# Performance work log

Measured on AMD Instinct MI355X. Metric: run time of the kernel, lower is better.

## Reference

```python
import jax, jax.numpy as jnp
import numpy as np

HID = 512
NUM_NODES = 100000
N_BATCH = 20000


def _gru_cell(x, h, W_ih, W_hh, b_ih, b_hh):
    # torch nn.GRU single-step cell; gate order r, z, n
    gi = x @ W_ih.T + b_ih            # [N, 3H]
    gh = h @ W_hh.T + b_hh            # [N, 3H]
    i_r, i_z, i_n = jnp.split(gi, 3, axis=-1)
    h_r, h_z, h_n = jnp.split(gh, 3, axis=-1)
    r = jax.nn.sigmoid(i_r + h_r)
    z = jax.nn.sigmoid(i_z + h_z)
    n = jnp.tanh(i_n + r * h_n)
    return (1.0 - z) * n + z * h


def setup_inputs() -> dict:
    key = jax.random.key(0)
    ks = jax.random.split(key, 12)
    s = 1.0 / np.sqrt(HID)
    inp = {
        'conv_emb': jax.random.normal(ks[0], (N_BATCH, HID), jnp.float32),
        'static_table': jax.random.normal(ks[1], (NUM_NODES, HID), jnp.float32),
        'dynamic_table': jax.random.normal(ks[2], (NUM_NODES, 2, HID), jnp.float32),
        'W_ih0': jax.random.normal(ks[3], (3 * HID, 2 * HID), jnp.float32) * s,
        'W_hh0': jax.random.normal(ks[4], (3 * HID, HID), jnp.float32) * s,
        'b_ih0': jax.random.normal(ks[5], (3 * HID,), jnp.float32) * s,
        'b_hh0': jax.random.normal(ks[6], (3 * HID,), jnp.float32) * s,
        'W_ih1': jax.random.normal(ks[7], (3 * HID, HID), jnp.float32) * s,
        'W_hh1': jax.random.normal(ks[8], (3 * HID, HID), jnp.float32) * s,
        'b_ih1': jax.random.normal(ks[9], (3 * HID,), jnp.float32) * s,
        'b_hh1': jax.random.normal(ks[10], (3 * HID,), jnp.float32) * s,
        'nids': jnp.arange(N_BATCH, dtype=jnp.int32),  # unique global node ids
    }
    return inp


def reference(conv_emb, static_table, dynamic_table,
              W_ih0, W_hh0, b_ih0, b_hh0,
              W_ih1, W_hh1, b_ih1, b_hh1, nids):
    # gather: static embeddings for batch nodes, concat with conv output
    x = jnp.concatenate([conv_emb, static_table[nids]], axis=-1)  # [N, 2H]
    h0 = dynamic_table[nids]                                      # [N, L, H]
    # single-step 2-layer GRU (seq_len == 1)
    h_new0 = _gru_cell(x, h0[:, 0], W_ih0, W_hh0, b_ih0, b_hh0)   # [N, H]
    h_new1 = _gru_cell(h_new0, h0[:, 1], W_ih1, W_hh1, b_ih1, b_hh1)
    hn = jnp.stack([h_new0, h_new1], axis=1)                      # [N, L, H]
    # scatter updated hidden states back into the persistent table
    updated_table = dynamic_table.at[nids].set(hn)                # [num_nodes, L, H]
    return updated_table
```

## Files before the change

### kernel.cpp

```cpp
#include <hip/hip_runtime.h>

#define NB 20000
#define NNODES 100000
#define MB2 79
#define MP2 (MB2*256)
#define NBITW 3125
#define NGEMM (MB2*8)

typedef unsigned short u16;
typedef __bf16 bf16x8 __attribute__((ext_vector_type(8)));
typedef float f32x4 __attribute__((ext_vector_type(4)));

__device__ __forceinline__ u16 f2bf(float f) {
  union { float f; unsigned u; } v; v.f = f;
  unsigned r = v.u + 0x7fffu + ((v.u >> 16) & 1u);
  return (u16)(r >> 16);
}
__device__ __forceinline__ float bf2f(u16 b) {
  union { unsigned u; float f; } v; v.u = ((unsigned)b) << 16;
  return v.f;
}

__global__ void prep_bt0i(const float* __restrict__ Wih, const float* __restrict__ Whh,
                          u16* __restrict__ Bt) {
  int idx = blockIdx.x * 256 + threadIdx.x;
  if (idx >= 2048 * 384) return;
  int jg = idx / 384;
  int k = (idx % 384) * 4;
  int j = jg >> 2, g = jg & 3;
  float4 v = make_float4(0.f, 0.f, 0.f, 0.f);
  if (g < 2) {
    int row = g * 512 + j;
    v = (k < 1024) ? *(const float4*)(Wih + (size_t)row * 1024 + k)
                   : *(const float4*)(Whh + (size_t)row * 512 + (k - 1024));
  } else if (g == 2) {
    if (k < 1024) v = *(const float4*)(Wih + (size_t)(1024 + j) * 1024 + k);
  } else {
    if (k >= 1024) v = *(const float4*)(Whh + (size_t)(1024 + j) * 512 + (k - 1024));
  }
  ushort4 b; b.x = f2bf(v.x); b.y = f2bf(v.y); b.z = f2bf(v.z); b.w = f2bf(v.w);
  *(ushort4*)(Bt + (size_t)jg * 1536 + k) = b;
}

__global__ void prep_bt1i(const float* __restrict__ Wih, const float* __restrict__ Whh,
                          u16* __restrict__ Bt) {
  int idx = blockIdx.x * 256 + threadIdx.x;
  if (idx >= 2048 * 256) return;
  int jg = idx / 256;
  int k = (idx % 256) * 4;
  int j = jg >> 2, g = jg & 3;
  float4 v = make_float4(0.f, 0.f, 0.f, 0.f);
  if (g < 2) {
    int row = g * 512 + j;
    v = (k < 512) ? *(const float4*)(Wih + (size_t)row * 512 + k)
                  : *(const float4*)(Whh + (size_t)row * 512 + (k - 512));
  } else if (g == 2) {
    if (k < 512) v = *(const float4*)(Wih + (size_t)(1024 + j) * 512 + k);
  } else {
    if (k >= 512) v = *(const float4*)(Whh + (size_t)(1024 + j) * 512 + (k - 512));
  }
  ushort4 b; b.x = f2bf(v.x); b.y = f2bf(v.y); b.z = f2bf(v.z); b.w = f2bf(v.w);
  *(ushort4*)(Bt + (size_t)jg * 1024 + k) = b;
}

__global__ void prep_a(const float* __restrict__ conv, const float* __restrict__ stat,
                       const float* __restrict__ dyn, const int* __restrict__ nids,
                       u16* __restrict__ A0, u16* __restrict__ A1) {
  int idx = blockIdx.x * 256 + threadIdx.x;
  int n = idx >> 9;
  int c = (idx & 511) * 4;
  if (n >= MP2) return;
  float4 v = make_float4(0.f, 0.f, 0.f, 0.f);
  if (n < NB) {
    size_t nid = (size_t)nids[n];
    if (c < 512)        v = *(const float4*)(conv + (size_t)n * 512 + c);
    else if (c < 1024)  v = *(const float4*)(stat + nid * 512 + (c - 512));
    else if (c < 1536)  v = *(const float4*)(dyn + nid * 1024 + (c - 1024));
    else                v = *(const float4*)(dyn + nid * 1024 + 512 + (c - 1536));
  }
  ushort4 b; b.x = f2bf(v.x); b.y = f2bf(v.y); b.z = f2bf(v.z); b.w = f2bf(v.w);
  if (c < 1536) *(ushort4*)(A0 + (size_t)n * 1536 + c) = b;
  else          *(ushort4*)(A1 + (size_t)n * 1024 + (c - 1024)) = b;
  if (n >= NB && c < 512) *(ushort4*)(A1 + (size_t)n * 1024 + c) = b;
}

__global__ void zero_bits(unsigned* __restrict__ bits) {
  int i = blockIdx.x * 256 + threadIdx.x;
  if (i < NBITW) bits[i] = 0;
}
__global__ void set_bits(const int* __restrict__ nids, unsigned* __restrict__ bits) {
  int i = blockIdx.x * 256 + threadIdx.x;
  if (i < NB) {
    int nid = nids[i];
    atomicOr(&bits[nid >> 5], 1u << (nid & 31));
  }
}

template <int K, int LAYER>
__global__ __launch_bounds__(512, 2)
void gemmt(const u16* __restrict__ A, const u16* __restrict__ Bt,
           const float* __restrict__ bih, const float* __restrict__ bhh,
           const u16* __restrict__ hsrc, int hstride, const int* __restrict__ nids,
           u16* __restrict__ a1out, float* __restrict__ out) {
  constexpr int NT = K / 64;
  __shared__ u16 S[2][2][2][8192];

  int bid = blockIdx.x;
  int bn = bid & 7, bm = bid >> 3;

  int t = threadIdx.x;
  int lane = t & 63, w = t >> 6;
  int fr = lane & 15, fq = lane >> 4;
  int wm = w >> 2, wn = w & 3;

  const u16* Ap = A + (size_t)bm * 256 * K;
  const u16* Bp = Bt + (size_t)bn * 256 * K;

  int srow[2], skc[2];
#pragma unroll
  for (int l = 0; l < 2; ++l) {
    int c = l * 512 + t;
    int p = c >> 4, up = c & 15;
    int u = up ^ ((p & 7) << 1);
    srow[l] = (p << 1) | (u & 1);
    skc[l] = u >> 1;
  }
  auto stage = [&](int kt) {
    char* base = (char*)S + (size_t)(kt & 1) * 65536;
#pragma unroll
    for (int m = 0; m < 2; ++m)
#pragma unroll
      for (int h = 0; h < 2; ++h)
#pragma unroll
        for (int l = 0; l < 2; ++l) {
          const u16* g = (m ? Bp : Ap) + (size_t)(h * 128 + srow[l]) * K + kt * 64 + skc[l] * 8;
          __builtin_amdgcn_global_load_lds(
              (const __attribute__((address_space(1))) void*)g,
              (__attribute__((address_space(3))) void*)
              (base + m * 32768 + h * 16384 + (l * 512 + t) * 16), 16, 0, 0);
        }
  };

  int swz = (((fr >> 1) & 7) << 1);
  int ub = ((fq << 1) | (fr & 1)) ^ swz;
  int offA[4], offA2[4], offB[4];
#pragma unroll
  for (int mi = 0; mi < 4; ++mi) {
    offA[mi]  = wm * 16384 + (mi * 8 + (fr >> 1)) * 256 + ub * 16;
    offA2[mi] = wm * 16384 + ((mi + 4) * 8 + (fr >> 1)) * 256 + ub * 16;
  }
#pragma unroll
  for (int nf = 0; nf < 4; ++nf)
    offB[nf] = 32768 + (wn >> 1) * 16384 +
               ((wn & 1) * 32 + nf * 8 + (fr >> 1)) * 256 + ub * 16;

  f32x4 acc[8][4] = {};

  stage(0);
  __syncthreads();

  for (int kt = 0; kt < NT; ++kt) {
    const char* sb = (const char*)S + (size_t)(kt & 1) * 65536;

    bf16x8 a0[4], b0[4], a1v[4];
#pragma unroll
    for (int mi = 0; mi < 4; ++mi) a0[mi] = *(const bf16x8*)(sb + offA[mi]);
#pragma unroll
    for (int nf = 0; nf < 4; ++nf) b0[nf] = *(const bf16x8*)(sb + offB[nf]);

    if (kt + 1 < NT) stage(kt + 1);

    __builtin_amdgcn_s_setprio(1);
#pragma unroll
    for (int mi = 0; mi < 4; ++mi)
#pragma unroll
      for (int nf = 0; nf < 4; ++nf)
        acc[mi][nf] = __builtin_amdgcn_mfma_f32_16x16x32_bf16(a0[mi], b0[nf],
                                                              acc[mi][nf], 0, 0, 0);
#pragma unroll
    for (int mi = 0; mi < 4; ++mi) a1v[mi] = *(const bf16x8*)(sb + offA2[mi]);
#pragma unroll
    for (int mi = 0; mi < 4; ++mi)
#pragma unroll
      for (int nf = 0; nf < 4; ++nf)
        acc[mi + 4][nf] = __builtin_amdgcn_mfma_f32_16x16x32_bf16(a1v[mi], b0[nf],
                                                                  acc[mi + 4][nf], 0, 0, 0);
#pragma unroll
    for (int mi = 0; mi < 4; ++mi) a0[mi] = *(const bf16x8*)(sb + (offA[mi] ^ 128));
#pragma unroll
    for (int nf = 0; nf < 4; ++nf) b0[nf] = *(const bf16x8*)(sb + (offB[nf] ^ 128));
#pragma unroll
    for (int mi = 0; mi < 4; ++mi)
#pragma unroll
      for (int nf = 0; nf < 4; ++nf)
        acc[mi][nf] = __builtin_amdgcn_mfma_f32_16x16x32_bf16(a0[mi], b0[nf],
                                                              acc[mi][nf], 0, 0, 0);
#pragma unroll
    for (int mi = 0; mi < 4; ++mi) a1v[mi] = *(const bf16x8*)(sb + (offA2[mi] ^ 128));
#pragma unroll
    for (int mi = 0; mi < 4; ++mi)
#pragma unroll
      for (int nf = 0; nf < 4; ++nf)
        acc[mi + 4][nf] = __builtin_amdgcn_mfma_f32_16x16x32_bf16(a1v[mi], b0[nf],
                                                                  acc[mi + 4][nf], 0, 0, 0);
    __builtin_amdgcn_s_setprio(0);

    __syncthreads();
  }

  int gg = fr & 3, jj = fr >> 2;
  const int jbase = bn * 64 + wn * 16;
  float bias[4];
#pragma unroll
  for (int nf = 0; nf < 4; ++nf) {
    int j = jbase + nf * 4 + jj;
    bias[nf] = (gg == 0) ? bih[j] + bhh[j]
             : (gg == 1) ? bih[512 + j] + bhh[512 + j]
             : (gg == 2) ? bih[1024 + j] : bhh[1024 + j];
  }
#pragma unroll
  for (int mi = 0; mi < 8; ++mi) {
    int row = bm * 256 + wm * 128 + mi * 16 + fq * 4 + gg;
    float zv[4], nv[4];
#pragma unroll
    for (int nf = 0; nf < 4; ++nf) {
      float v[4], v1[4], v2[4];
#pragma unroll
      for (int r = 0; r < 4; ++r) v[r] = acc[mi][nf][r] + bias[nf];
#pragma unroll
      for (int i = 0; i < 4; ++i) {
        float o = __shfl_xor(v[i ^ 2], 2);
        v1[i] = ((i ^ gg) & 2) ? o : v[i];
      }
#pragma unroll
      for (int i = 0; i < 4; ++i) {
        float o = __shfl_xor(v1[i ^ 1], 1);
        v2[i] = ((i ^ gg) & 1) ? o : v1[i];
      }
      float rr = 1.f / (1.f + __expf(-v2[0]));
      zv[nf] = 1.f / (1.f + __expf(-v2[1]));
      nv[nf] = tanhf(fmaf(rr, v2[3], v2[2]));
    }
    float z1[4], z2[4], n1[4], n2[4];
#pragma unroll
    for (int i = 0; i < 4; ++i) {
      float oz = __shfl_xor(zv[i ^ 2], 8);
      float on = __shfl_xor(nv[i ^ 2], 8);
      z1[i] = ((i ^ jj) & 2) ? oz : zv[i];
      n1[i] = ((i ^ jj) & 2) ? on : nv[i];
    }
#pragma unroll
    for (int i = 0; i < 4; ++i) {
      float oz = __shfl_xor(z1[i ^ 1], 4);
      float on = __shfl_xor(n1[i ^ 1], 4);
      z2[i] = ((i ^ jj) & 1) ? oz : z1[i];
      n2[i] = ((i ^ jj) & 1) ? on : n1[i];
    }
    if (row < NB) {
      int j4 = jbase + jj * 4;
      ushort4 hv = *(const ushort4*)(hsrc + (size_t)row * hstride + j4);
      float hp0 = fmaf(z2[0], bf2f(hv.x) - n2[0], n2[0]);
      float hp1 = fmaf(z2[1], bf2f(hv.y) - n2[1], n2[1]);
      float hp2 = fmaf(z2[2], bf2f(hv.z) - n2[2], n2[2]);
      float hp3 = fmaf(z2[3], bf2f(hv.w) - n2[3], n2[3]);
      size_t nid = (size_t)nids[row];
      *(float4*)(out + nid * 1024 + LAYER * 512 + j4) = make_float4(hp0, hp1, hp2, hp3);
      if (LAYER == 0) {
        ushort4 ob; ob.x = f2bf(hp0); ob.y = f2bf(hp1); ob.z = f2bf(hp2); ob.w = f2bf(hp3);
        *(ushort4*)(a1out + (size_t)row * 1024 + j4) = ob;
      }
    }
  }
}

__global__ void copy_skip(const float4* __restrict__ src, float4* __restrict__ dst,
                          const unsigned* __restrict__ bits) {
  const size_t total = (size_t)NNODES * 256;
  for (size_t i = (size_t)blockIdx.x * 256 + threadIdx.x; i < total;
       i += (size_t)gridDim.x * 256) {
    int row = (int)(i >> 8);
    if (!((bits[row >> 5] >> (row & 31)) & 1u)) {
      dst[i] = src[i];
    }
  }
}

extern "C" void kernel_launch(void* const* d_in, const int* in_sizes, int n_in,
                              void* d_out, int out_size, void* d_ws, size_t ws_size,
                              hipStream_t stream) {
  const float* conv = (const float*)d_in[0];
  const float* stat = (const float*)d_in[1];
  const float* dyn  = (const float*)d_in[2];
  const float* Wih0 = (const float*)d_in[3];
  const float* Whh0 = (const float*)d_in[4];
  const float* bih0 = (const float*)d_in[5];
  const float* bhh0 = (const float*)d_in[6];
  const float* Wih1 = (const float*)d_in[7];
  const float* Whh1 = (const float*)d_in[8];
  const float* bih1 = (const float*)d_in[9];
  const float* bhh1 = (const float*)d_in[10];
  const int*   nids = (const int*)d_in[11];
  float* out = (float*)d_out;

  char* ws = (char*)d_ws;
  u16* A0  = (u16*)ws;
  u16* A1  = (u16*)(ws + 62128128);
  u16* Bt0 = (u16*)(ws + 103546880);
  u16* Bt1 = (u16*)(ws + 109838336);
  unsigned* bits = (unsigned*)(ws + 114032640);

  zero_bits<<<(NBITW + 255) / 256, 256, 0, stream>>>(bits);
  set_bits<<<(NB + 255) / 256, 256, 0, stream>>>(nids, bits);
  prep_bt0i<<<3072, 256, 0, stream>>>(Wih0, Whh0, Bt0);
  prep_bt1i<<<2048, 256, 0, stream>>>(Wih1, Whh1, Bt1);
  prep_a<<<(MP2 * 512) / 256, 256, 0, stream>>>(conv, stat, dyn, nids, A0, A1);

  gemmt<1536, 0><<<NGEMM, 512, 0, stream>>>(A0, Bt0, bih0, bhh0,
                                            A0 + 1024, 1536, nids, A1, out);
  gemmt<1024, 1><<<NGEMM, 512, 0, stream>>>(A1, Bt1, bih1, bhh1,
                                            A1 + 512, 1024, nids, (u16*)nullptr, out);

  copy_skip<<<2048, 256, 0, stream>>>((const float4*)dyn, (float4*)out, bits);
}
```

Baseline: 496.8 us.

## Shrink GEMM tiles to 128x128 with 256 threads and XCD-aware block remap

Reworks the fused GRU GEMM kernels from 256x256 tiles on 512 threads to 128x128 tiles on 256 threads. LDS per block is halved and the grid grows from 632 to 2528 blocks, for better load balance and occupancy across CUs. Block indices are also remapped so consecutive blocks on one XCD share A/B panels, improving L2 reuse. Smaller tiles lower arithmetic intensity and increase global and LDS traffic per flop.

After: 529.3 us. 6.5% more time.

```diff
diff --git a/kernel.cpp b/kernel.cpp
--- a/kernel.cpp
+++ b/kernel.cpp
@@ -2,10 +2,11 @@
 
 #define NB 20000
 #define NNODES 100000
-#define MB2 79
-#define MP2 (MB2*256)
+#define MP2 20224
 #define NBITW 3125
-#define NGEMM (MB2*8)
+#define MBG 158
+#define NBN 16
+#define NGEMM (MBG*NBN)
 
 typedef unsigned short u16;
 typedef __bf16 bf16x8 __attribute__((ext_vector_type(8)));
@@ -97,72 +98,71 @@
 }
 
 template <int K, int LAYER>
-__global__ __launch_bounds__(512, 2)
+__global__ __launch_bounds__(256, 2)
 void gemmt(const u16* __restrict__ A, const u16* __restrict__ Bt,
            const float* __restrict__ bih, const float* __restrict__ bhh,
            const u16* __restrict__ hsrc, int hstride, const int* __restrict__ nids,
            u16* __restrict__ a1out, float* __restrict__ out) {
   constexpr int NT = K / 64;
-  __shared__ u16 S[2][2][2][8192];
+  __shared__ u16 S[2][2][8192];
 
   int bid = blockIdx.x;
-  int bn = bid & 7, bm = bid >> 3;
+  int gidx = (bid & 7) * (NGEMM / 8) + (bid >> 3);
+  int bn = gidx / MBG, bm = gidx - bn * MBG;
 
   int t = threadIdx.x;
   int lane = t & 63, w = t >> 6;
   int fr = lane & 15, fq = lane >> 4;
-  int wm = w >> 2, wn = w & 3;
-
-  const u16* Ap = A + (size_t)bm * 256 * K;
-  const u16* Bp = Bt + (size_t)bn * 256 * K;
-
-  int srow[2], skc[2];
-#pragma unroll
-  for (int l = 0; l < 2; ++l) {
-    int c = l * 512 + t;
-    int p = c >> 4, up = c & 15;
+  int wr = w >> 1, wc = w & 1;
+
+  const u16* Ap = A + (size_t)bm * 128 * K;
+  const u16* Bp = Bt + (size_t)bn * 128 * K;
+
+  int goff[8], gsel[8];
+#pragma unroll
+  for (int l = 0; l < 8; ++l) {
+    int c = l * 256 + t;
+    gsel[l] = c >> 10;
+    int cm = c & 1023;
+    int p = cm >> 4, up = cm & 15;
     int u = up ^ ((p & 7) << 1);
-    srow[l] = (p << 1) | (u & 1);
-    skc[l] = u >> 1;
+    goff[l] = (2 * p + (u & 1)) * K + (u >> 1) * 8;
   }
   auto stage = [&](int kt) {
-    char* base = (char*)S + (size_t)(kt & 1) * 65536;
-#pragma unroll
-    for (int m = 0; m < 2; ++m)
-#pragma unroll
-      for (int h = 0; h < 2; ++h)
-#pragma unroll
-        for (int l = 0; l < 2; ++l) {
-          const u16* g = (m ? Bp : Ap) + (size_t)(h * 128 + srow[l]) * K + kt * 64 + skc[l] * 8;
-          __builtin_amdgcn_global_load_lds(
-              (const __attribute__((address_space(1))) void*)g,
-              (__attribute__((address_space(3))) void*)
-              (base + m * 32768 + h * 16384 + (l * 512 + t) * 16), 16, 0, 0);
-        }
+    char* base = (char*)S + (size_t)(kt & 1) * 32768;
+#pragma unroll
+    for (int l = 0; l < 8; ++l) {
+      const u16* g = (gsel[l] ? Bp : Ap) + goff[l] + kt * 64;
+      __builtin_amdgcn_global_load_lds(
+          (const __attribute__((address_space(1))) void*)g,
+          (__attribute__((address_space(3))) void*)
+          (base + (l * 256 + t) * 16), 16, 0, 0);
+    }
   };
 
-  int swz = (((fr >> 1) & 7) << 1);
-  int ub = ((fq << 1) | (fr & 1)) ^ swz;
-  int offA[4], offA2[4], offB[4];
+  int offA[4], offB[4];
 #pragma unroll
   for (int mi = 0; mi < 4; ++mi) {
-    offA[mi]  = wm * 16384 + (mi * 8 + (fr >> 1)) * 256 + ub * 16;
-    offA2[mi] = wm * 16384 + ((mi + 4) * 8 + (fr >> 1)) * 256 + ub * 16;
-  }
-#pragma unroll
-  for (int nf = 0; nf < 4; ++nf)
-    offB[nf] = 32768 + (wn >> 1) * 16384 +
-               ((wn & 1) * 32 + nf * 8 + (fr >> 1)) * 256 + ub * 16;
-
-  f32x4 acc[8][4] = {};
+    int p = wr * 32 + mi * 8 + (fr >> 1);
+    int u = ((fq << 1) | (fr & 1)) ^ ((p & 7) << 1);
+    offA[mi] = p * 256 + u * 16;
+  }
+#pragma unroll
+  for (int nf = 0; nf < 4; ++nf) {
+    int p = wc * 32 + nf * 8 + (fr >> 1);
+    int u = ((fq << 1) | (fr & 1)) ^ ((p & 7) << 1);
+    offB[nf] = 16384 + p * 256 + u * 16;
+  }
+
+  f32x4 acc[4][4] = {};
 
   stage(0);
   __syncthreads();
 
   for (int kt = 0; kt < NT; ++kt) {
-    const char* sb = (const char*)S + (size_t)(kt & 1) * 65536;
-
-    bf16x8 a0[4], b0[4], a1v[4];
+    const char* sb = (const char*)S + (size_t)(kt & 1) * 32768;
+
+    bf16x8 a0[4], b0[4];
 #pragma unroll
     for (int mi = 0; mi < 4; ++mi) a0[mi] = *(const bf16x8*)(sb + offA[mi]);
 #pragma unroll
@@ -178,14 +178,6 @@
         acc[mi][nf] = __builtin_amdgcn_mfma_f32_16x16x32_bf16(a0[mi], b0[nf],
                                                               acc[mi][nf], 0, 0, 0);
 #pragma unroll
-    for (int mi = 0; mi < 4; ++mi) a1v[mi] = *(const bf16x8*)(sb + offA2[mi]);
-#pragma unroll
-    for (int mi = 0; mi < 4; ++mi)
-#pragma unroll
-      for (int nf = 0; nf < 4; ++nf)
-        acc[mi + 4][nf] = __builtin_amdgcn_mfma_f32_16x16x32_bf16(a1v[mi], b0[nf],
-                                                                  acc[mi + 4][nf], 0, 0, 0);
-#pragma unroll
     for (int mi = 0; mi < 4; ++mi) a0[mi] = *(const bf16x8*)(sb + (offA[mi] ^ 128));
 #pragma unroll
     for (int nf = 0; nf < 4; ++nf) b0[nf] = *(const bf16x8*)(sb + (offB[nf] ^ 128));
@@ -195,21 +187,13 @@
       for (int nf = 0; nf < 4; ++nf)
         acc[mi][nf] = __builtin_amdgcn_mfma_f32_16x16x32_bf16(a0[mi], b0[nf],
                                                               acc[mi][nf], 0, 0, 0);
-#pragma unroll
-    for (int mi = 0; mi < 4; ++mi) a1v[mi] = *(const bf16x8*)(sb + (offA2[mi] ^ 128));
-#pragma unroll
-    for (int mi = 0; mi < 4; ++mi)
-#pragma unroll
-      for (int nf = 0; nf < 4; ++nf)
-        acc[mi + 4][nf] = __builtin_amdgcn_mfma_f32_16x16x32_bf16(a1v[mi], b0[nf],
-                                                                  acc[mi + 4][nf], 0, 0, 0);
     __builtin_amdgcn_s_setprio(0);
 
     __syncthreads();
   }
 
   int gg = fr & 3, jj = fr >> 2;
-  const int jbase = bn * 64 + wn * 16;
+  const int jbase = bn * 32 + wc * 16;
   float bias[4];
 #pragma unroll
   for (int nf = 0; nf < 4; ++nf) {
@@ -219,8 +203,8 @@
              : (gg == 2) ? bih[1024 + j] : bhh[1024 + j];
   }
 #pragma unroll
-  for (int mi = 0; mi < 8; ++mi) {
-    int row = bm * 256 + wm * 128 + mi * 16 + fq * 4 + gg;
+  for (int mi = 0; mi < 4; ++mi) {
+    int row = bm * 128 + wr * 64 + mi * 16 + fq * 4 + gg;
     float zv[4], nv[4];
 #pragma unroll
     for (int nf = 0; nf < 4; ++nf) {
@@ -315,9 +299,9 @@
   prep_bt1i<<<2048, 256, 0, stream>>>(Wih1, Whh1, Bt1);
   prep_a<<<(MP2 * 512) / 256, 256, 0, stream>>>(conv, stat, dyn, nids, A0, A1);
 
-  gemmt<1536, 0><<<NGEMM, 512, 0, stream>>>(A0, Bt0, bih0, bhh0,
+  gemmt<1536, 0><<<NGEMM, 256, 0, stream>>>(A0, Bt0, bih0, bhh0,
                                             A0 + 1024, 1536, nids, A1, out);
-  gemmt<1024, 1><<<NGEMM, 512, 0, stream>>>(A1, Bt1, bih1, bhh1,
+  gemmt<1024, 1><<<NGEMM, 256, 0, stream>>>(A1, Bt1, bih1, bhh1,
                                             A1 + 512, 1024, nids, (u16*)nullptr, out);
 
   copy_skip<<<2048, 256, 0, stream>>>((const float4*)dyn, (float4*)out, bits);
```

## Fuse skip-row table copy into GEMM kernels as interleaved copy blocks

Applied to the files above, without the earlier changes.

Removes the separate copy_skip kernel and instead assigns every third block of each GRU-layer GEMM launch to copy the unchanged rows of the dynamic table, splitting the rows between the two launches. The memory-bound copy is meant to overlap with the compute-bound GEMM and drop one kernel launch. The copy now uses nontemporal loads and stores with 8-way unrolling. In exchange, the copy blocks compete with GEMM blocks for bandwidth and CU slots, and the grid grows.

Result: slower. 567.5 us (+14.2%).

```diff
diff --git a/kernel.cpp b/kernel.cpp
--- a/kernel.cpp
+++ b/kernel.cpp
@@ -6,6 +6,8 @@
 #define MP2 (MB2*256)
 #define NBITW 3125
 #define NGEMM (MB2*8)
+#define NCOPY 316
+#define GRID (NGEMM + NCOPY)
 
 typedef unsigned short u16;
 typedef __bf16 bf16x8 __attribute__((ext_vector_type(8)));
@@ -101,14 +103,40 @@
 void gemmt(const u16* __restrict__ A, const u16* __restrict__ Bt,
            const float* __restrict__ bih, const float* __restrict__ bhh,
            const u16* __restrict__ hsrc, int hstride, const int* __restrict__ nids,
-           u16* __restrict__ a1out, float* __restrict__ out) {
+           u16* __restrict__ a1out, float* __restrict__ out,
+           const f32x4* __restrict__ src4, f32x4* __restrict__ dst4,
+           const unsigned* __restrict__ bits, long cbase, long climit, int cper) {
   constexpr int NT = K / 64;
   __shared__ u16 S[2][2][2][8192];
 
-  int bid = blockIdx.x;
+  int bid0 = blockIdx.x;
+  int t = threadIdx.x;
+
+  if (bid0 % 3 == 2) {
+    int cb = bid0 / 3;
+    long s = cbase + (long)cb * cper;
+    long e = s + cper; if (e > climit) e = climit;
+    for (long i = s + t; i < e; i += 512L * 8) {
+      f32x4 v[8]; int ok[8];
+#pragma unroll
+      for (int u = 0; u < 8; ++u) {
+        long ix = i + (long)u * 512;
+        int row = (int)(ix >> 8);
+        ok[u] = (ix < e) && !((bits[row >> 5] >> (row & 31)) & 1u);
+        if (ok[u]) v[u] = __builtin_nontemporal_load(&src4[ix]);
+      }
+#pragma unroll
+      for (int u = 0; u < 8; ++u) {
+        long ix = i + (long)u * 512;
+        if (ok[u]) __builtin_nontemporal_store(v[u], &dst4[ix]);
+      }
+    }
+    return;
+  }
+  int bid = bid0 - (bid0 + 1) / 3;
+
   int bn = bid & 7, bm = bid >> 3;
 
-  int t = threadIdx.x;
   int lane = t & 63, w = t >> 6;
   int fr = lane & 15, fq = lane >> 4;
   int wm = w >> 2, wn = w & 3;
@@ -269,18 +297,6 @@
         ushort4 ob; ob.x = f2bf(hp0); ob.y = f2bf(hp1); ob.z = f2bf(hp2); ob.w = f2bf(hp3);
         *(ushort4*)(a1out + (size_t)row * 1024 + j4) = ob;
       }
-    }
-  }
-}
-
-__global__ void copy_skip(const float4* __restrict__ src, float4* __restrict__ dst,
-                          const unsigned* __restrict__ bits) {
-  const size_t total = (size_t)NNODES * 256;
-  for (size_t i = (size_t)blockIdx.x * 256 + threadIdx.x; i < total;
-       i += (size_t)gridDim.x * 256) {
-    int row = (int)(i >> 8);
-    if (!((bits[row >> 5] >> (row & 31)) & 1u)) {
-      dst[i] = src[i];
     }
   }
 }
@@ -315,10 +331,16 @@
   prep_bt1i<<<2048, 256, 0, stream>>>(Wih1, Whh1, Bt1);
   prep_a<<<(MP2 * 512) / 256, 256, 0, stream>>>(conv, stat, dyn, nids, A0, A1);
 
-  gemmt<1536, 0><<<NGEMM, 512, 0, stream>>>(A0, Bt0, bih0, bhh0,
-                                            A0 + 1024, 1536, nids, A1, out);
-  gemmt<1024, 1><<<NGEMM, 512, 0, stream>>>(A1, Bt1, bih1, bhh1,
-                                            A1 + 512, 1024, nids, (u16*)nullptr, out);
-
-  copy_skip<<<2048, 256, 0, stream>>>((const float4*)dyn, (float4*)out, bits);
-}
+  const long C0 = 60000L * 256, C1 = 100000L * 256;
+  const int per0 = (int)((C0 + NCOPY - 1) / NCOPY);
+  const int per1 = (int)((C1 - C0 + NCOPY - 1) / NCOPY);
+
+  gemmt<1536, 0><<<GRID, 512, 0, stream>>>(A0, Bt0, bih0, bhh0,
+                                           A0 + 1024, 1536, nids, A1, out,
+                                           (const f32x4*)dyn, (f32x4*)out, bits,
+                                           0L, C0, per0);
+  gemmt<1024, 1><<<GRID, 512, 0, stream>>>(A1, Bt1, bih1, bhh1,
+                                           A1 + 512, 1024, nids, (u16*)nullptr, out,
+                                           (const f32x4*)dyn, (f32x4*)out, bits,
+                                           C0, C1, per1);
+}
```
